# Performance work log

Hardware: AMD Instinct MI355X
Metric: run time of the kernel (lower is better)

Reference implementation:

```python
import jax, jax.numpy as jnp
import numpy as np

A, B, I, H, O = 400, 64, 50, 192, 3   # num_agents, batch, input_dim, hidden_dim, output_dim
ADIM, NH = 128, 8                      # attention_dim, num_heads
HD = ADIM // NH
SCALE = HD ** -0.5
EPS = 1e-5


def _ln(x, g, b):
    mu = jnp.mean(x, -1, keepdims=True)
    v = jnp.mean((x - mu) ** 2, -1, keepdims=True)
    return (x - mu) * jax.lax.rsqrt(v + EPS) * g + b


def setup_inputs() -> dict:
    key = jax.random.key(0)
    ks = jax.random.split(key, 12)
    s = 0.05
    n = lambda k, shape: (jax.random.normal(k, shape, jnp.float32) * s)
    return {
        'x': jax.random.normal(ks[0], (B, I), jnp.float32),
        'ln_in_g': jnp.ones((A, I), jnp.float32), 'ln_in_b': jnp.zeros((A, I), jnp.float32),
        'W1': n(ks[1], (A, I, H)), 'b1': jnp.zeros((A, H), jnp.float32),
        'Ws1': n(ks[2], (A, I, H)), 'bs1': jnp.zeros((A, H), jnp.float32),
        'W2': n(ks[3], (A, H, H)), 'b2': jnp.zeros((A, H), jnp.float32),
        'Ws2': n(ks[4], (A, H, H)), 'bs2': jnp.zeros((A, H), jnp.float32),
        'W3': n(ks[5], (A, H, H)), 'b3': jnp.zeros((A, H), jnp.float32),
        'ln_h_g': jnp.ones((A, H), jnp.float32), 'ln_h_b': jnp.zeros((A, H), jnp.float32),
        'Wout': n(ks[6], (A, H, O)), 'bout': jnp.zeros((A, O), jnp.float32),
        'aln_g': jnp.ones((H,), jnp.float32), 'aln_b': jnp.zeros((H,), jnp.float32),
        'Wq': n(ks[7], (H, ADIM)), 'bq': jnp.zeros((ADIM,), jnp.float32),
        'Wk': n(ks[8], (H, ADIM)), 'bk': jnp.zeros((ADIM,), jnp.float32),
        'Wv': n(ks[9], (H, ADIM)), 'bv': jnp.zeros((ADIM,), jnp.float32),
        'Wo': n(ks[10], (ADIM, H)), 'bo': jnp.zeros((H,), jnp.float32),
    }


def _forward(x, ln_in_g, ln_in_b, W1, b1, Ws1, bs1, W2, b2, Ws2, bs2, W3, b3,
             ln_h_g, ln_h_b, Wout, bout, aln_g, aln_b, Wq, bq, Wk, bk, Wv, bv, Wo, bo):
    gelu = lambda t: jax.nn.gelu(t, approximate=False)  # torch F.gelu default = exact erf
    # per-agent input LayerNorm (shared stats, per-agent affine) -> [A, B, I]
    xn = _ln(x[None, :, :], ln_in_g[:, None, :], ln_in_b[:, None, :])
    # agent MLPs as batched GEMMs over agent axis
    h1 = gelu(jnp.einsum('abi,aih->abh', xn, W1) + b1[:, None, :]) \
         + jnp.einsum('abi,aih->abh', xn, Ws1) + bs1[:, None, :]
    h2 = gelu(jnp.einsum('abh,ahk->abk', h1, W2) + b2[:, None, :]) \
         + jnp.einsum('abh,ahk->abk', h1, Ws2) + bs2[:, None, :]
    h3 = _ln(h2 + jnp.einsum('abh,ahk->abk', h2, W3) + b3[:, None, :],
             ln_h_g[:, None, :], ln_h_b[:, None, :])  # [A, B, H]
    # cross-SREK attention across the agent axis
    y = _ln(h3, aln_g, aln_b)
    q = (y @ Wq + bq).reshape(A, B, NH, HD).transpose(1, 2, 0, 3)  # [B, NH, A, HD]
    k = (y @ Wk + bk).reshape(A, B, NH, HD).transpose(1, 2, 0, 3)
    v = (y @ Wv + bv).reshape(A, B, NH, HD).transpose(1, 2, 0, 3)
    attn = jax.nn.softmax(jnp.einsum('bhad,bhcd->bhac', q, k) * SCALE, axis=-1)
    o = jnp.einsum('bhac,bhcd->bhad', attn, v).transpose(2, 0, 1, 3).reshape(A, B, ADIM)
    attended = h3 + (o @ Wo + bo)  # residual (dropout off in eval)
    # per-agent output heads -> [A, B, O]
    logits = jnp.einsum('abh,aho->abo', attended, Wout) + bout[:, None, :]
    return logits


def reference(x, ln_in_g, ln_in_b, W1, b1, Ws1, bs1, W2, b2, Ws2, bs2, W3, b3,
              ln_h_g, ln_h_b, Wout, bout, aln_g, aln_b, Wq, bq, Wk, bk, Wv, bv, Wo, bo):
    return _forward(x, ln_in_g, ln_in_b, W1, b1, Ws1, bs1, W2, b2, Ws2, bs2, W3, b3,
                    ln_h_g, ln_h_b, Wout, bout, aln_g, aln_b, Wq, bq, Wk, bk, Wv, bv, Wo, bo)
```

## Files before the change

### kernel.cpp

```cpp
#include <hip/hip_runtime.h>
#include <math.h>

#define AGENTS 400
#define BATCH  64
#define IDIM   50
#define HDIM   192
#define ODIM   3
#define ADIMM  128
#define NHEADS 8
#define HEADD  16
#define LN_EPS 1e-5f

#define PA   200
#define PWK  40
#define POUT 136

typedef __bf16 bf16x8 __attribute__((ext_vector_type(8)));
typedef float  f32x4  __attribute__((ext_vector_type(4)));

__device__ __forceinline__ float gelu_exact(float x) {
    return 0.5f * x * (1.0f + erff(x * 0.70710678118654752f));
}

__device__ __forceinline__ unsigned pack_bf16x2(float a, float b) {
    unsigned short ua = __builtin_bit_cast(unsigned short, (__bf16)a);
    unsigned short ub = __builtin_bit_cast(unsigned short, (__bf16)b);
    return (unsigned)ua | ((unsigned)ub << 16);
}

__device__ __forceinline__ void stage_w(__bf16* Wtb, const float* __restrict__ Wg,
                                        int kc, int kd, int wave, int lane)
{
    #pragma unroll
    for (int i = 0; i < 4; i++) {
        int kp = (i << 2) + wave;
        int k0 = kc + (kp << 1);
        #pragma unroll
        for (int j = 0; j < 3; j++) {
            int n = lane + (j << 6);
            float f0 = (k0     < kd) ? Wg[(size_t)k0 * HDIM + n]       : 0.f;
            float f1 = (k0 + 1 < kd) ? Wg[(size_t)(k0 + 1) * HDIM + n] : 0.f;
            *(unsigned*)&Wtb[n * PWK + (kp << 1)] = pack_bf16x2(f0, f1);
        }
    }
}

__device__ __forceinline__ void slot_mfma(f32x4 (&acc)[4][3], const __bf16* As_,
                                          const __bf16* Wtb, int kofs, int n0, int lane)
{
    const int r = lane & 15, g = lane >> 4;
    bf16x8 bf[3];
    #pragma unroll
    for (int t = 0; t < 3; t++)
        bf[t] = *(const bf16x8*)&Wtb[(n0 + 16 * t + r) * PWK + g * 8];
    #pragma unroll
    for (int rg = 0; rg < 4; rg++) {
        bf16x8 af = *(const bf16x8*)&As_[(16 * rg + r) * PA + kofs + g * 8];
        #pragma unroll
        for (int t = 0; t < 3; t++)
            acc[rg][t] = __builtin_amdgcn_mfma_f32_16x16x32_bf16(af, bf[t], acc[rg][t], 0, 0, 0);
    }
}

__global__ __launch_bounds__(256, 2) void mlp_kernel(
    const float* __restrict__ x,
    const float* __restrict__ ln_in_g, const float* __restrict__ ln_in_b,
    const float* __restrict__ W1, const float* __restrict__ b1,
    const float* __restrict__ Ws1, const float* __restrict__ bs1,
    const float* __restrict__ W2, const float* __restrict__ b2,
    const float* __restrict__ Ws2, const float* __restrict__ bs2,
    const float* __restrict__ W3, const float* __restrict__ b3,
    const float* __restrict__ ln_h_g, const float* __restrict__ ln_h_b,
    float* __restrict__ h3out)
{
    const int a    = blockIdx.x;
    const int tid  = threadIdx.x;
    const int wave = tid >> 6, lane = tid & 63;
    const int r = lane & 15, g = lane >> 4;
    const int n0 = 48 * wave;

    __shared__ __align__(16) __bf16 As[64 * PA];
    __shared__ __align__(16) __bf16 Wt[2][192 * PWK];
    __shared__ float mu_s[64], rs_s[64];

    {
        int rr = tid >> 2, l = tid & 3;
        float s = 0.f, ss = 0.f;
        for (int k = l; k < IDIM; k += 4) { float v = x[rr * IDIM + k]; s += v; ss += v * v; }
        s  += __shfl_down(s, 2, 4);  s  += __shfl_down(s, 1, 4);
        ss += __shfl_down(ss, 2, 4); ss += __shfl_down(ss, 1, 4);
        if (l == 0) {
            float mu = s * (1.0f / IDIM);
            float var = ss * (1.0f / IDIM) - mu * mu;
            mu_s[rr] = mu;
            rs_s[rr] = rsqrtf(var + LN_EPS);
        }
    }
    __syncthreads();
    for (int sidx = tid; sidx < 64 * 64; sidx += 256) {
        int rr = sidx >> 6, k = sidx & 63;
        float v = 0.f;
        if (k < IDIM)
            v = (x[rr * IDIM + k] - mu_s[rr]) * rs_s[rr] * ln_in_g[a * IDIM + k] + ln_in_b[a * IDIM + k];
        As[rr * PA + k] = (__bf16)v;
    }
    __syncthreads();

    const float* W1p  = W1  + (size_t)a * IDIM * HDIM;
    const float* Ws1p = Ws1 + (size_t)a * IDIM * HDIM;
    const float* W2p  = W2  + (size_t)a * HDIM * HDIM;
    const float* Ws2p = Ws2 + (size_t)a * HDIM * HDIM;
    const float* W3p  = W3  + (size_t)a * HDIM * HDIM;

    {
        f32x4 acc1[4][3], acc2[4][3];
        #pragma unroll
        for (int i = 0; i < 4; i++)
            #pragma unroll
            for (int t = 0; t < 3; t++) { acc1[i][t] = (f32x4)0.f; acc2[i][t] = (f32x4)0.f; }
        stage_w(Wt[0], W1p, 0, IDIM, wave, lane);
        __syncthreads();
        #pragma unroll
        for (int s = 0; s < 4; s++) {
            if (s + 1 < 4) {
                int ns = s + 1;
                stage_w(Wt[(s + 1) & 1], (ns & 1) ? Ws1p : W1p, (ns >> 1) * 32, IDIM, wave, lane);
            }
            if ((s & 1) == 0) slot_mfma(acc1, As, Wt[s & 1], (s >> 1) * 32, n0, lane);
            else              slot_mfma(acc2, As, Wt[s & 1], (s >> 1) * 32, n0, lane);
            __syncthreads();
        }
        #pragma unroll
        for (int t = 0; t < 3; t++) {
            int col = n0 + 16 * t + r;
            float bb  = b1[a * HDIM + col];
            float bbs = bs1[a * HDIM + col];
            #pragma unroll
            for (int rg = 0; rg < 4; rg++)
                #pragma unroll
                for (int i = 0; i < 4; i++) {
                    int row = 16 * rg + 4 * g + i;
                    As[row * PA + col] = (__bf16)(gelu_exact(acc1[rg][t][i] + bb) + acc2[rg][t][i] + bbs);
                }
        }
        __syncthreads();
    }

    {
        f32x4 acc1[4][3], acc2[4][3];
        #pragma unroll
        for (int i = 0; i < 4; i++)
            #pragma unroll
            for (int t = 0; t < 3; t++) { acc1[i][t] = (f32x4)0.f; acc2[i][t] = (f32x4)0.f; }
        stage_w(Wt[0], W2p, 0, HDIM, wave, lane);
        __syncthreads();
        #pragma unroll
        for (int s = 0; s < 12; s++) {
            if (s + 1 < 12) {
                int ns = s + 1;
                stage_w(Wt[(s + 1) & 1], (ns & 1) ? Ws2p : W2p, (ns >> 1) * 32, HDIM, wave, lane);
            }
            if ((s & 1) == 0) slot_mfma(acc1, As, Wt[s & 1], (s >> 1) * 32, n0, lane);
            else              slot_mfma(acc2, As, Wt[s & 1], (s >> 1) * 32, n0, lane);
            __syncthreads();
        }
        #pragma unroll
        for (int t = 0; t < 3; t++) {
            int col = n0 + 16 * t + r;
            float bb  = b2[a * HDIM + col];
            float bbs = bs2[a * HDIM + col];
            #pragma unroll
            for (int rg = 0; rg < 4; rg++)
                #pragma unroll
                for (int i = 0; i < 4; i++) {
                    int row = 16 * rg + 4 * g + i;
                    As[row * PA + col] = (__bf16)(gelu_exact(acc1[rg][t][i] + bb) + acc2[rg][t][i] + bbs);
                }
        }
        __syncthreads();
    }

    {
        f32x4 acc[4][3];
        #pragma unroll
        for (int i = 0; i < 4; i++)
            #pragma unroll
            for (int t = 0; t < 3; t++) acc[i][t] = (f32x4)0.f;
        stage_w(Wt[0], W3p, 0, HDIM, wave, lane);
        __syncthreads();
        #pragma unroll
        for (int s = 0; s < 6; s++) {
            if (s + 1 < 6)
                stage_w(Wt[(s + 1) & 1], W3p, (s + 1) * 32, HDIM, wave, lane);
            slot_mfma(acc, As, Wt[s & 1], s * 32, n0, lane);
            __syncthreads();
        }
        #pragma unroll
        for (int t = 0; t < 3; t++) {
            int col = n0 + 16 * t + r;
            float bb = b3[a * HDIM + col];
            #pragma unroll
            for (int rg = 0; rg < 4; rg++)
                #pragma unroll
                for (int i = 0; i < 4; i++) {
                    int row = 16 * rg + 4 * g + i;
                    As[row * PA + col] = (__bf16)((float)As[row * PA + col] + acc[rg][t][i] + bb);
                }
        }
        __syncthreads();
    }

    {
        int rr = tid >> 2, l = tid & 3;
        float s = 0.f, ss = 0.f;
        for (int k = l; k < HDIM; k += 4) { float v = (float)As[rr * PA + k]; s += v; ss += v * v; }
        s  += __shfl_down(s, 2, 4);  s  += __shfl_down(s, 1, 4);
        ss += __shfl_down(ss, 2, 4); ss += __shfl_down(ss, 1, 4);
        if (l == 0) {
            float mu = s * (1.0f / HDIM);
            float var = ss * (1.0f / HDIM) - mu * mu;
            mu_s[rr] = mu;
            rs_s[rr] = rsqrtf(var + LN_EPS);
        }
    }
    __syncthreads();
    for (int sidx = tid; sidx < 64 * HDIM; sidx += 256) {
        int rr = sidx / HDIM, c = sidx - rr * HDIM;
        float v = ((float)As[rr * PA + c] - mu_s[rr]) * rs_s[rr] * ln_h_g[a * HDIM + c] + ln_h_b[a * HDIM + c];
        h3out[((size_t)a * BATCH + rr) * HDIM + c] = v;
    }
}

template<int NC, int KD, int NT, int NRG, int LDW, int PITCH>
__device__ __forceinline__ void gemm_bpass(f32x4 (&acc)[NRG][NT],
                                           const float* const* wptr,
                                           const __bf16* Asrc, int lane)
{
    const int r = lane & 15, g = lane >> 4;
    float buf[2][NT * 8];

    #pragma unroll
    for (int t = 0; t < NT; t++)
        #pragma unroll
        for (int j = 0; j < 8; j++) {
            int k = g * 8 + j;
            buf[0][t * 8 + j] = (k < KD) ? wptr[t][k * LDW + r] : 0.f;
        }

    #pragma unroll
    for (int c = 0; c < NC; c++) {
        const int cur = c & 1, nxt = cur ^ 1;
        if (c + 1 < NC) {
            #pragma unroll
            for (int t = 0; t < NT; t++)
                #pragma unroll
                for (int j = 0; j < 8; j++) {
                    int k = (c + 1) * 32 + g * 8 + j;
                    buf[nxt][t * 8 + j] = (k < KD) ? wptr[t][k * LDW + r] : 0.f;
                }
        }
        bf16x8 bfr[NT];
        #pragma unroll
        for (int t = 0; t < NT; t++)
            #pragma unroll
            for (int j = 0; j < 8; j++)
                bfr[t][j] = (__bf16)buf[cur][t * 8 + j];
        #pragma unroll
        for (int rg = 0; rg < NRG; rg++) {
            bf16x8 af = *(const bf16x8*)&Asrc[(16 * rg + r) * PITCH + c * 32 + g * 8];
            #pragma unroll
            for (int t = 0; t < NT; t++)
                acc[rg][t] = __builtin_amdgcn_mfma_f32_16x16x32_bf16(af, bfr[t], acc[rg][t], 0, 0, 0);
        }
    }
}

__global__ __launch_bounds__(256, 2) void qkv_kernel(
    const float* __restrict__ h3,
    const float* __restrict__ aln_g, const float* __restrict__ aln_b,
    const float* __restrict__ Wq, const float* __restrict__ bq,
    const float* __restrict__ Wk, const float* __restrict__ bk,
    const float* __restrict__ Wv, const float* __restrict__ bv,
    float* __restrict__ qT, float* __restrict__ kT, float* __restrict__ vT)
{
    const int a    = blockIdx.x;
    const int tid  = threadIdx.x;
    const int wave = tid >> 6, lane = tid & 63;
    const int r = lane & 15, g = lane >> 4;

    __shared__ __align__(16) __bf16 ys[64 * PA];
    __shared__ float mu_s[64], rs_s[64];

    {
        int rr = tid >> 2, l = tid & 3;
        const float* hp = h3 + ((size_t)a * BATCH + rr) * HDIM;
        float s = 0.f, ss = 0.f;
        for (int k = l; k < HDIM; k += 4) { float v = hp[k]; s += v; ss += v * v; }
        s  += __shfl_down(s, 2, 4);  s  += __shfl_down(s, 1, 4);
        ss += __shfl_down(ss, 2, 4); ss += __shfl_down(ss, 1, 4);
        if (l == 0) {
            float mu = s * (1.0f / HDIM);
            float var = ss * (1.0f / HDIM) - mu * mu;
            mu_s[rr] = mu;
            rs_s[rr] = rsqrtf(var + LN_EPS);
        }
    }
    __syncthreads();
    for (int sidx = tid; sidx < 64 * HDIM; sidx += 256) {
        int rr = sidx / HDIM, c = sidx - rr * HDIM;
        float v = (h3[((size_t)a * BATCH + rr) * HDIM + c] - mu_s[rr]) * rs_s[rr] * aln_g[c] + aln_b[c];
        ys[rr * PA + c] = (__bf16)v;
    }
    __syncthreads();

    #pragma unroll
    for (int p = 0; p < 2; p++) {
        const int nb = 192 * p + 48 * wave;
        const float* wA[3];
        #pragma unroll
        for (int t = 0; t < 3; t++) {
            int nt = nb + 16 * t;
            const float* base = (nt < 128) ? Wq : (nt < 256) ? Wk : Wv;
            wA[t] = base + (nt & 127);
        }
        f32x4 acc[4][3];
        #pragma unroll
        for (int i = 0; i < 4; i++)
            #pragma unroll
            for (int t = 0; t < 3; t++) acc[i][t] = (f32x4)0.f;
        gemm_bpass<6, HDIM, 3, 4, ADIMM, PA>(acc, wA, ys, lane);

        #pragma unroll
        for (int t = 0; t < 3; t++) {
            int n = nb + 16 * t + r;
            int which = n >> 7, cc = n & 127, hh = cc >> 4, dd = cc & 15;
            const float* bp = (which == 0) ? bq : (which == 1) ? bk : bv;
            float* op = (which == 0) ? qT : (which == 1) ? kT : vT;
            float bb = bp[cc];
            #pragma unroll
            for (int rg = 0; rg < 4; rg++)
                #pragma unroll
                for (int i = 0; i < 4; i++) {
                    int brow = 16 * rg + 4 * g + i;
                    op[(((size_t)brow * NHEADS + hh) * AGENTS + a) * HEADD + dd] = acc[rg][t][i] + bb;
                }
        }
    }
}

#define PKA 24
#define PVA 408
#define PPA 232

__global__ __launch_bounds__(256, 2) void attn_kernel(
    const float* __restrict__ qT, const float* __restrict__ kT,
    const float* __restrict__ vT, float* __restrict__ oT)
{
    const int bh   = blockIdx.x;
    const int b    = bh >> 3, h = bh & 7;
    const int tid  = threadIdx.x;
    const int wave = tid >> 6, lane = tid & 63;
    const int r = lane & 15, g = lane >> 4;

    __shared__ __align__(16) __bf16 Ks[AGENTS * PKA];
    __shared__ __align__(16) __bf16 Vt[16 * PVA];
    __shared__ __align__(16) __bf16 Ps[4][16 * PPA];

    const float* kp = kT + (size_t)bh * AGENTS * HEADD;
    const float* vp = vT + (size_t)bh * AGENTS * HEADD;
    for (int idx = tid; idx < AGENTS * HEADD; idx += 256) {
        int a_ = idx >> 4, d = idx & 15;
        Ks[a_ * PKA + d] = (__bf16)kp[idx];
        Vt[d * PVA + a_] = (__bf16)vp[idx];
    }
    __bf16* Pw = Ps[wave];
    for (int z = lane; z < 16 * 16; z += 64)
        Pw[(z >> 4) * PPA + 208 + (z & 15)] = (__bf16)0.f;
    __syncthreads();

    for (int mt = wave; mt < 25; mt += 4) {
        const int m0 = mt * 16;

        bf16x8 aq;
        if (g < 2) {
            const float* qp = qT + ((size_t)bh * AGENTS + m0 + r) * HEADD + g * 8;
            #pragma unroll
            for (int j = 0; j < 8; j++) aq[j] = (__bf16)(qp[j] * 0.25f);
        } else {
            #pragma unroll
            for (int j = 0; j < 8; j++) aq[j] = (__bf16)0.f;
        }

        f32x4 sacc[25];
        #pragma unroll
        for (int t = 0; t < 25; t++) {
            bf16x8 bk_ = *(const bf16x8*)&Ks[(t * 16 + r) * PKA + (g & 1) * 8];
            sacc[t] = __builtin_amdgcn_mfma_f32_16x16x32_bf16(aq, bk_, (f32x4)0.f, 0, 0, 0);
        }

        float lv[4];
        #pragma unroll
        for (int i = 0; i < 4; i++) {
            float m_ = sacc[0][i];
            #pragma unroll
            for (int t = 1; t < 25; t++) m_ = fmaxf(m_, sacc[t][i]);
            #pragma unroll
            for (int off = 8; off; off >>= 1) m_ = fmaxf(m_, __shfl_xor(m_, off, 16));
            float l_ = 0.f;
            #pragma unroll
            for (int t = 0; t < 25; t++) {
                float p = __expf(sacc[t][i] - m_);
                sacc[t][i] = p;
                l_ += p;
            }
            #pragma unroll
            for (int off = 8; off; off >>= 1) l_ += __shfl_xor(l_, off, 16);
            lv[i] = l_;
        }

        f32x4 oacc = (f32x4)0.f;

        #pragma unroll
        for (int t = 0; t < 13; t++)
            #pragma unroll
            for (int i = 0; i < 4; i++)
                Pw[(g * 4 + i) * PPA + t * 16 + r] = (__bf16)sacc[t][i];
        __asm__ volatile("s_waitcnt lgkmcnt(0)" ::: "memory");
        #pragma unroll
        for (int c = 0; c < 7; c++) {
            bf16x8 ap  = *(const bf16x8*)&Pw[r * PPA + c * 32 + g * 8];
            bf16x8 bv_ = *(const bf16x8*)&Vt[r * PVA + c * 32 + g * 8];
            oacc = __builtin_amdgcn_mfma_f32_16x16x32_bf16(ap, bv_, oacc, 0, 0, 0);
        }

        for (int z = lane; z < 16 * 16; z += 64)
            Pw[(z >> 4) * PPA + 192 + (z & 15)] = (__bf16)0.f;
        #pragma unroll
        for (int t = 13; t < 25; t++)
            #pragma unroll
            for (int i = 0; i < 4; i++)
                Pw[(g * 4 + i) * PPA + (t - 13) * 16 + r] = (__bf16)sacc[t][i];
        __asm__ volatile("s_waitcnt lgkmcnt(0)" ::: "memory");
        #pragma unroll
        for (int c = 0; c < 6; c++) {
            bf16x8 ap  = *(const bf16x8*)&Pw[r * PPA + c * 32 + g * 8];
            bf16x8 bv_ = *(const bf16x8*)&Vt[r * PVA + 208 + c * 32 + g * 8];
            oacc = __builtin_amdgcn_mfma_f32_16x16x32_bf16(ap, bv_, oacc, 0, 0, 0);
        }

        #pragma unroll
        for (int i = 0; i < 4; i++)
            oT[((size_t)(m0 + g * 4 + i) * BATCH + b) * ADIMM + h * HEADD + r] = oacc[i] / lv[i];
    }
}

__global__ __launch_bounds__(256, 2) void out_kernel(
    const float* __restrict__ h3, const float* __restrict__ oT,
    const float* __restrict__ Wo, const float* __restrict__ bo,
    const float* __restrict__ Wout, const float* __restrict__ bout,
    float* __restrict__ out)
{
    const int a    = blockIdx.x;
    const int tid  = threadIdx.x;
    const int wave = tid >> 6, lane = tid & 63;
    const int r = lane & 15, g = lane >> 4;
    const int n0 = 48 * wave;

    __shared__ __align__(16) __bf16 os[64 * POUT];
    __shared__ __align__(16) __bf16 att[64 * PA];

    for (int idx = tid; idx < 64 * 32; idx += 256) {
        int bb = idx >> 5, q = idx & 31;
        float4 v = ((const float4*)(oT + ((size_t)a * BATCH + bb) * ADIMM))[q];
        unsigned u0 = pack_bf16x2(v.x, v.y);
        unsigned u1 = pack_bf16x2(v.z, v.w);
        *(uint2*)&os[bb * POUT + q * 4] = make_uint2(u0, u1);
    }
    __syncthreads();

    {
        const float* wA[3] = { Wo + n0, Wo + n0 + 16, Wo + n0 + 32 };
        f32x4 acc[4][3];
        #pragma unroll
        for (int i = 0; i < 4; i++)
            #pragma unroll
            for (int t = 0; t < 3; t++) acc[i][t] = (f32x4)0.f;
        gemm_bpass<4, ADIMM, 3, 4, HDIM, POUT>(acc, wA, os, lane);
        #pragma unroll
        for (int t = 0; t < 3; t++) {
            int col = n0 + 16 * t + r;
            float bb = bo[col];
            #pragma unroll
            for (int rg = 0; rg < 4; rg++)
                #pragma unroll
                for (int i = 0; i < 4; i++) {
                    int row = 16 * rg + 4 * g + i;
                    float v = h3[((size_t)a * BATCH + row) * HDIM + col] + acc[rg][t][i] + bb;
                    att[row * PA + col] = (__bf16)v;
                }
        }
    }
    __syncthreads();

    {
        const float* Wp = Wout + (size_t)a * HDIM * ODIM;
        float wb[48];
        #pragma unroll
        for (int c = 0; c < 6; c++)
            #pragma unroll
            for (int j = 0; j < 8; j++) {
                int k = c * 32 + g * 8 + j;
                wb[c * 8 + j] = (r < ODIM) ? Wp[k * ODIM + r] : 0.f;
            }
        f32x4 oacc = (f32x4)0.f;
        #pragma unroll
        for (int c = 0; c < 6; c++) {
            bf16x8 bf;
            #pragma unroll
            for (int j = 0; j < 8; j++) bf[j] = (__bf16)wb[c * 8 + j];
            bf16x8 af = *(const bf16x8*)&att[(16 * wave + r) * PA + c * 32 + g * 8];
            oacc = __builtin_amdgcn_mfma_f32_16x16x32_bf16(af, bf, oacc, 0, 0, 0);
        }
        if (r < ODIM) {
            float bb = bout[a * ODIM + r];
            #pragma unroll
            for (int i = 0; i < 4; i++) {
                int row = 16 * wave + 4 * g + i;
                out[((size_t)a * BATCH + row) * ODIM + r] = oacc[i] + bb;
            }
        }
    }
}

extern "C" void kernel_launch(void* const* d_in, const int* in_sizes, int n_in,
                              void* d_out, int out_size, void* d_ws, size_t ws_size,
                              hipStream_t stream)
{
    const float* x       = (const float*)d_in[0];
    const float* ln_in_g = (const float*)d_in[1];
    const float* ln_in_b = (const float*)d_in[2];
    const float* W1      = (const float*)d_in[3];
    const float* b1      = (const float*)d_in[4];
    const float* Ws1     = (const float*)d_in[5];
    const float* bs1     = (const float*)d_in[6];
    const float* W2      = (const float*)d_in[7];
    const float* b2      = (const float*)d_in[8];
    const float* Ws2     = (const float*)d_in[9];
    const float* bs2     = (const float*)d_in[10];
    const float* W3      = (const float*)d_in[11];
    const float* b3      = (const float*)d_in[12];
    const float* ln_h_g  = (const float*)d_in[13];
    const float* ln_h_b  = (const float*)d_in[14];
    const float* Wout    = (const float*)d_in[15];
    const float* bout    = (const float*)d_in[16];
    const float* aln_g   = (const float*)d_in[17];
    const float* aln_b   = (const float*)d_in[18];
    const float* Wq      = (const float*)d_in[19];
    const float* bq      = (const float*)d_in[20];
    const float* Wk      = (const float*)d_in[21];
    const float* bk      = (const float*)d_in[22];
    const float* Wv      = (const float*)d_in[23];
    const float* bv      = (const float*)d_in[24];
    const float* Wo      = (const float*)d_in[25];
    const float* bo      = (const float*)d_in[26];
    float* out = (float*)d_out;

    float* ws = (float*)d_ws;
    const size_t H3_SZ = (size_t)AGENTS * BATCH * HDIM;
    const size_t QT_SZ = (size_t)BATCH * NHEADS * AGENTS * HEADD;
    float* h3 = ws;
    float* qT = h3 + H3_SZ;
    float* kT = qT + QT_SZ;
    float* vT = kT + QT_SZ;
    float* oT = vT + QT_SZ;

    mlp_kernel<<<AGENTS, 256, 0, stream>>>(x, ln_in_g, ln_in_b,
                                           W1, b1, Ws1, bs1, W2, b2, Ws2, bs2,
                                           W3, b3, ln_h_g, ln_h_b, h3);
    qkv_kernel<<<AGENTS, 256, 0, stream>>>(h3, aln_g, aln_b,
                                           Wq, bq, Wk, bk, Wv, bv, qT, kT, vT);
    attn_kernel<<<BATCH * NHEADS, 256, 0, stream>>>(qT, kT, vT, oT);
    out_kernel<<<AGENTS, 256, 0, stream>>>(h3, oT, Wo, bo, Wout, bout, out);
}
```

Measured before the change: 386.1 us.

## Load MLP weights directly into registers and drop LDS weight staging

The shared-memory double-buffered weight staging and its per-slot barriers are removed. Each wave now loads its own B-fragment weights from global memory into registers, with a one-chunk register prefetch. The activation tile switches to an unpadded XOR-swizzled layout to avoid bank conflicts, and the final LayerNorm store is vectorised with float4. This removes LDS traffic and many __syncthreads, at the cost of higher register pressure and global loads that are strided across K rather than coalesced.

```diff
diff --git a/kernel.cpp b/kernel.cpp
--- a/kernel.cpp
+++ b/kernel.cpp
@@ -12,7 +12,7 @@
 #define LN_EPS 1e-5f
 
 #define PA   200
-#define PWK  40
+#define PAM  192
 #define POUT 136
 
 typedef __bf16 bf16x8 __attribute__((ext_vector_type(8)));
@@ -28,37 +28,114 @@
     return (unsigned)ua | ((unsigned)ub << 16);
 }
 
-__device__ __forceinline__ void stage_w(__bf16* Wtb, const float* __restrict__ Wg,
-                                        int kc, int kd, int wave, int lane)
-{
-    #pragma unroll
-    for (int i = 0; i < 4; i++) {
-        int kp = (i << 2) + wave;
-        int k0 = kc + (kp << 1);
-        #pragma unroll
-        for (int j = 0; j < 3; j++) {
-            int n = lane + (j << 6);
-            float f0 = (k0     < kd) ? Wg[(size_t)k0 * HDIM + n]       : 0.f;
-            float f1 = (k0 + 1 < kd) ? Wg[(size_t)(k0 + 1) * HDIM + n] : 0.f;
-            *(unsigned*)&Wtb[n * PWK + (kp << 1)] = pack_bf16x2(f0, f1);
-        }
-    }
-}
-
-__device__ __forceinline__ void slot_mfma(f32x4 (&acc)[4][3], const __bf16* As_,
-                                          const __bf16* Wtb, int kofs, int n0, int lane)
+__device__ __forceinline__ int as_swz(int row, int col) {
+    return ((((col >> 3) ^ (row & 7)) << 3) | (col & 7));
+}
+__device__ __forceinline__ void st_as(__bf16* As_, int row, int col, float v) {
+    As_[row * PAM + as_swz(row, col)] = (__bf16)v;
+}
+__device__ __forceinline__ float ld_as(const __bf16* As_, int row, int col) {
+    return (float)As_[row * PAM + as_swz(row, col)];
+}
+__device__ __forceinline__ bf16x8 ld_afrag(const __bf16* As_, int row, int k0) {
+    int blk = (((k0 >> 3) ^ (row & 7)) << 3);
+    return *(const bf16x8*)&As_[row * PAM + blk];
+}
+
+template<int NC, int KD>
+__device__ __forceinline__ void mlp_gemm2(f32x4 (&acc1)[4][3], f32x4 (&acc2)[4][3],
+                                          const float* __restrict__ W,
+                                          const float* __restrict__ Ws,
+                                          const __bf16* As_, int n0, int lane)
 {
     const int r = lane & 15, g = lane >> 4;
-    bf16x8 bf[3];
+    const int colb[3] = { n0 + r, n0 + 16 + r, n0 + 32 + r };
+    float b1f[24], b2f[24];
+
     #pragma unroll
     for (int t = 0; t < 3; t++)
-        bf[t] = *(const bf16x8*)&Wtb[(n0 + 16 * t + r) * PWK + g * 8];
+        #pragma unroll
+        for (int j = 0; j < 8; j++) {
+            int k = g * 8 + j;
+            int off = k * HDIM + colb[t];
+            b1f[t * 8 + j] = (k < KD) ? W[off]  : 0.f;
+            b2f[t * 8 + j] = (k < KD) ? Ws[off] : 0.f;
+        }
+
     #pragma unroll
-    for (int rg = 0; rg < 4; rg++) {
-        bf16x8 af = *(const bf16x8*)&As_[(16 * rg + r) * PA + kofs + g * 8];
+    for (int c = 0; c < NC; c++) {
+        bf16x8 bf1[3], bf2[3];
         #pragma unroll
         for (int t = 0; t < 3; t++)
-            acc[rg][t] = __builtin_amdgcn_mfma_f32_16x16x32_bf16(af, bf[t], acc[rg][t], 0, 0, 0);
+            #pragma unroll
+            for (int j = 0; j < 8; j++) {
+                bf1[t][j] = (__bf16)b1f[t * 8 + j];
+                bf2[t][j] = (__bf16)b2f[t * 8 + j];
+            }
+        if (c + 1 < NC) {
+            #pragma unroll
+            for (int t = 0; t < 3; t++)
+                #pragma unroll
+                for (int j = 0; j < 8; j++) {
+                    int k = (c + 1) * 32 + g * 8 + j;
+                    int off = k * HDIM + colb[t];
+                    b1f[t * 8 + j] = (k < KD) ? W[off]  : 0.f;
+                    b2f[t * 8 + j] = (k < KD) ? Ws[off] : 0.f;
+                }
+        }
+        #pragma unroll
+        for (int rg = 0; rg < 4; rg++) {
+            bf16x8 af = ld_afrag(As_, 16 * rg + r, c * 32 + g * 8);
+            #pragma unroll
+            for (int t = 0; t < 3; t++) {
+                acc1[rg][t] = __builtin_amdgcn_mfma_f32_16x16x32_bf16(af, bf1[t], acc1[rg][t], 0, 0, 0);
+                acc2[rg][t] = __builtin_amdgcn_mfma_f32_16x16x32_bf16(af, bf2[t], acc2[rg][t], 0, 0, 0);
+            }
+        }
+    }
+}
+
+template<int NC, int KD>
+__device__ __forceinline__ void mlp_gemm1(f32x4 (&acc)[4][3],
+                                          const float* __restrict__ W,
+                                          const __bf16* As_, int n0, int lane)
+{
+    const int r = lane & 15, g = lane >> 4;
+    const int colb[3] = { n0 + r, n0 + 16 + r, n0 + 32 + r };
+    float bf[24];
+
+    #pragma unroll
+    for (int t = 0; t < 3; t++)
+        #pragma unroll
+        for (int j = 0; j < 8; j++) {
+            int k = g * 8 + j;
+            bf[t * 8 + j] = (k < KD) ? W[k * HDIM + colb[t]] : 0.f;
+        }
+
+    #pragma unroll
+    for (int c = 0; c < NC; c++) {
+        bf16x8 bfr[3];
+        #pragma unroll
+        for (int t = 0; t < 3; t++)
+            #pragma unroll
+            for (int j = 0; j < 8; j++)
+                bfr[t][j] = (__bf16)bf[t * 8 + j];
+        if (c + 1 < NC) {
+            #pragma unroll
+            for (int t = 0; t < 3; t++)
+                #pragma unroll
+                for (int j = 0; j < 8; j++) {
+                    int k = (c + 1) * 32 + g * 8 + j;
+                    bf[t * 8 + j] = (k < KD) ? W[k * HDIM + colb[t]] : 0.f;
+                }
+        }
+        #pragma unroll
+        for (int rg = 0; rg < 4; rg++) {
+            bf16x8 af = ld_afrag(As_, 16 * rg + r, c * 32 + g * 8);
+            #pragma unroll
+            for (int t = 0; t < 3; t++)
+                acc[rg][t] = __builtin_amdgcn_mfma_f32_16x16x32_bf16(af, bfr[t], acc[rg][t], 0, 0, 0);
+        }
     }
 }
 
@@ -79,8 +156,7 @@
     const int r = lane & 15, g = lane >> 4;
     const int n0 = 48 * wave;
 
-    __shared__ __align__(16) __bf16 As[64 * PA];
-    __shared__ __align__(16) __bf16 Wt[2][192 * PWK];
+    __shared__ __align__(16) __bf16 As[64 * PAM];
     __shared__ float mu_s[64], rs_s[64];
 
     {
@@ -102,7 +178,7 @@
         float v = 0.f;
         if (k < IDIM)
             v = (x[rr * IDIM + k] - mu_s[rr]) * rs_s[rr] * ln_in_g[a * IDIM + k] + ln_in_b[a * IDIM + k];
-        As[rr * PA + k] = (__bf16)v;
+        st_as(As, rr, k, v);
     }
     __syncthreads();
 
@@ -118,18 +194,8 @@
         for (int i = 0; i < 4; i++)
             #pragma unroll
             for (int t = 0; t < 3; t++) { acc1[i][t] = (f32x4)0.f; acc2[i][t] = (f32x4)0.f; }
-        stage_w(Wt[0], W1p, 0, IDIM, wave, lane);
+        mlp_gemm2<2, IDIM>(acc1, acc2, W1p, Ws1p, As, n0, lane);
         __syncthreads();
-        #pragma unroll
-        for (int s = 0; s < 4; s++) {
-            if (s + 1 < 4) {
-                int ns = s + 1;
-                stage_w(Wt[(s + 1) & 1], (ns & 1) ? Ws1p : W1p, (ns >> 1) * 32, IDIM, wave, lane);
-            }
-            if ((s & 1) == 0) slot_mfma(acc1, As, Wt[s & 1], (s >> 1) * 32, n0, lane);
-            else              slot_mfma(acc2, As, Wt[s & 1], (s >> 1) * 32, n0, lane);
-            __syncthreads();
-        }
         #pragma unroll
         for (int t = 0; t < 3; t++) {
             int col = n0 + 16 * t + r;
@@ -140,7 +206,7 @@
                 #pragma unroll
                 for (int i = 0; i < 4; i++) {
                     int row = 16 * rg + 4 * g + i;
-                    As[row * PA + col] = (__bf16)(gelu_exact(acc1[rg][t][i] + bb) + acc2[rg][t][i] + bbs);
+                    st_as(As, row, col, gelu_exact(acc1[rg][t][i] + bb) + acc2[rg][t][i] + bbs);
                 }
         }
         __syncthreads();
@@ -152,18 +218,8 @@
         for (int i = 0; i < 4; i++)
             #pragma unroll
             for (int t = 0; t < 3; t++) { acc1[i][t] = (f32x4)0.f; acc2[i][t] = (f32x4)0.f; }
-        stage_w(Wt[0], W2p, 0, HDIM, wave, lane);
+        mlp_gemm2<6, HDIM>(acc1, acc2, W2p, Ws2p, As, n0, lane);
         __syncthreads();
-        #pragma unroll
-        for (int s = 0; s < 12; s++) {
-            if (s + 1 < 12) {
-                int ns = s + 1;
-                stage_w(Wt[(s + 1) & 1], (ns & 1) ? Ws2p : W2p, (ns >> 1) * 32, HDIM, wave, lane);
-            }
-            if ((s & 1) == 0) slot_mfma(acc1, As, Wt[s & 1], (s >> 1) * 32, n0, lane);
-            else              slot_mfma(acc2, As, Wt[s & 1], (s >> 1) * 32, n0, lane);
-            __syncthreads();
-        }
         #pragma unroll
         for (int t = 0; t < 3; t++) {
             int col = n0 + 16 * t + r;
@@ -174,7 +230,7 @@
                 #pragma unroll
                 for (int i = 0; i < 4; i++) {
                     int row = 16 * rg + 4 * g + i;
-                    As[row * PA + col] = (__bf16)(gelu_exact(acc1[rg][t][i] + bb) + acc2[rg][t][i] + bbs);
+                    st_as(As, row, col, gelu_exact(acc1[rg][t][i] + bb) + acc2[rg][t][i] + bbs);
                 }
         }
         __syncthreads();
@@ -186,15 +242,8 @@
         for (int i = 0; i < 4; i++)
             #pragma unroll
             for (int t = 0; t < 3; t++) acc[i][t] = (f32x4)0.f;
-        stage_w(Wt[0], W3p, 0, HDIM, wave, lane);
+        mlp_gemm1<6, HDIM>(acc, W3p, As, n0, lane);
         __syncthreads();
-        #pragma unroll
-        for (int s = 0; s < 6; s++) {
-            if (s + 1 < 6)
-                stage_w(Wt[(s + 1) & 1], W3p, (s + 1) * 32, HDIM, wave, lane);
-            slot_mfma(acc, As, Wt[s & 1], s * 32, n0, lane);
-            __syncthreads();
-        }
         #pragma unroll
         for (int t = 0; t < 3; t++) {
             int col = n0 + 16 * t + r;
@@ -204,7 +253,7 @@
                 #pragma unroll
                 for (int i = 0; i < 4; i++) {
                     int row = 16 * rg + 4 * g + i;
-                    As[row * PA + col] = (__bf16)((float)As[row * PA + col] + acc[rg][t][i] + bb);
+                    st_as(As, row, col, ld_as(As, row, col) + acc[rg][t][i] + bb);
                 }
         }
         __syncthreads();
@@ -213,7 +262,7 @@
     {
         int rr = tid >> 2, l = tid & 3;
         float s = 0.f, ss = 0.f;
-        for (int k = l; k < HDIM; k += 4) { float v = (float)As[rr * PA + k]; s += v; ss += v * v; }
+        for (int k = l; k < HDIM; k += 4) { float v = ld_as(As, rr, k); s += v; ss += v * v; }
         s  += __shfl_down(s, 2, 4);  s  += __shfl_down(s, 1, 4);
         ss += __shfl_down(ss, 2, 4); ss += __shfl_down(ss, 1, 4);
         if (l == 0) {
@@ -224,10 +273,19 @@
         }
     }
     __syncthreads();
-    for (int sidx = tid; sidx < 64 * HDIM; sidx += 256) {
-        int rr = sidx / HDIM, c = sidx - rr * HDIM;
-        float v = ((float)As[rr * PA + c] - mu_s[rr]) * rs_s[rr] * ln_h_g[a * HDIM + c] + ln_h_b[a * HDIM + c];
-        h3out[((size_t)a * BATCH + rr) * HDIM + c] = v;
+    for (int sidx = tid; sidx < 64 * 48; sidx += 256) {
+        int rr = sidx / 48, q = sidx - rr * 48;
+        int c = q * 4;
+        const __bf16* p = &As[rr * PAM + as_swz(rr, c)];
+        float4 gv = *(const float4*)&ln_h_g[a * HDIM + c];
+        float4 bv = *(const float4*)&ln_h_b[a * HDIM + c];
+        float mu = mu_s[rr], rs = rs_s[rr];
+        float4 o;
+        o.x = ((float)p[0] - mu) * rs * gv.x + bv.x;
+        o.y = ((float)p[1] - mu) * rs * gv.y + bv.y;
+        o.z = ((float)p[2] - mu) * rs * gv.z + bv.z;
+        o.w = ((float)p[3] - mu) * rs * gv.w + bv.w;
+        *(float4*)&h3out[((size_t)a * BATCH + rr) * HDIM + c] = o;
     }
 }
 
```

Measured after the change: 409.9 us. 6.2% more time.
